# Kernel optimization log

Hardware: AMD Instinct MI355X
Metric: run time of the kernel (lower is better)

## Reference

```python
import jax, jax.numpy as jnp
import numpy as np

VOCAB = 256
H = 4096
N_LAYERS = 2


def setup_inputs() -> dict:
    key = jax.random.key(0)
    ks = jax.random.split(key, 16)
    s = 1.0 / np.sqrt(H)
    inp = jax.random.randint(ks[0], (1,), 0, VOCAB)
    hidden = jax.random.normal(ks[1], (N_LAYERS, 1, H), dtype=jnp.float32)
    emb = jax.random.normal(ks[2], (VOCAB, H), dtype=jnp.float32)
    def u(k, shape):
        return jax.random.uniform(k, shape, jnp.float32, -s, s)
    return {
        'inp': inp,
        'hidden': hidden,
        'emb': emb,
        'W_ih0': u(ks[3], (3 * H, H)), 'W_hh0': u(ks[4], (3 * H, H)),
        'b_ih0': u(ks[5], (3 * H,)),   'b_hh0': u(ks[6], (3 * H,)),
        'W_ih1': u(ks[7], (3 * H, H)), 'W_hh1': u(ks[8], (3 * H, H)),
        'b_ih1': u(ks[9], (3 * H,)),   'b_hh1': u(ks[10], (3 * H,)),
        'W_dec': u(ks[11], (VOCAB, H)), 'b_dec': u(ks[12], (VOCAB,)),
    }


def _gru_cell(x, h, W_ih, W_hh, b_ih, b_hh):
    # x, h: [1, H]; PyTorch GRU gate math (gate order r, z, n)
    gi = x @ W_ih.T + b_ih  # [1, 3H]
    gh = h @ W_hh.T + b_hh  # [1, 3H]
    i_r, i_z, i_n = jnp.split(gi, 3, axis=-1)
    h_r, h_z, h_n = jnp.split(gh, 3, axis=-1)
    r = jax.nn.sigmoid(i_r + h_r)
    z = jax.nn.sigmoid(i_z + h_z)
    n = jnp.tanh(i_n + r * h_n)
    return (1.0 - z) * n + z * h


def reference(inp, hidden, emb, W_ih0, W_hh0, b_ih0, b_hh0,
              W_ih1, W_hh1, b_ih1, b_hh1, W_dec, b_dec):
    x = emb[inp]  # [1, H] embedding lookup (encoder)
    params = ((W_ih0, W_hh0, b_ih0, b_hh0), (W_ih1, W_hh1, b_ih1, b_hh1))
    new_h = []
    for l in range(N_LAYERS):
        h = _gru_cell(x, hidden[l], *params[l])  # [1, H]
        new_h.append(h)
        x = h  # output of layer l feeds layer l+1
    output = x @ W_dec.T + b_dec  # [1, VOCAB]
    return output, jnp.stack(new_h, axis=0)
```

## Files before the change

kernel.cpp:

```cpp
#include <hip/hip_runtime.h>

#define H 4096
#define NVOCAB 256

__device__ __forceinline__ float row_dot(const float* __restrict__ wrow,
                                         const float* __restrict__ vec,
                                         int lane) {
    const float4* wr = reinterpret_cast<const float4*>(wrow);
    const float4* xr = reinterpret_cast<const float4*>(vec);
    float acc = 0.f;
#pragma unroll
    for (int it = 0; it < 16; ++it) {
        int idx = it * 64 + lane;
        float4 w = wr[idx];
        float4 x = xr[idx];
        acc += w.x * x.x + w.y * x.y + w.z * x.z + w.w * x.w;
    }
#pragma unroll
    for (int off = 32; off > 0; off >>= 1) acc += __shfl_down(acc, off, 64);
    return acc;
}

__global__ __launch_bounds__(384) void gru_layer_kernel(
    const float* __restrict__ Wih,
    const float* __restrict__ Whh,
    const float* __restrict__ bih,
    const float* __restrict__ bhh,
    const float* __restrict__ xbase,
    const int* __restrict__ inp, int use_inp,
    const float* __restrict__ hprev,
    float* __restrict__ hout)
{
    __shared__ float lds[6];
    const int wave = threadIdx.x >> 6;
    const int lane = threadIdx.x & 63;
    const int i    = blockIdx.x;

    const float* x = xbase + (use_inp ? (size_t)inp[0] * H : 0);
    const int g = (wave < 3) ? wave : (wave - 3);
    const float* W    = (wave < 3) ? Wih : Whh;
    const float* vec  = (wave < 3) ? x   : hprev;
    const float* bias = (wave < 3) ? bih : bhh;

    float acc = row_dot(W + (size_t)(g * H + i) * H, vec, lane);
    if (lane == 0) lds[wave] = acc + bias[g * H + i];
    __syncthreads();

    if (threadIdx.x == 0) {
        float ir = lds[0], iz = lds[1], inn = lds[2];
        float hr = lds[3], hz = lds[4], hn  = lds[5];
        float r = 1.f / (1.f + __expf(-(ir + hr)));
        float z = 1.f / (1.f + __expf(-(iz + hz)));
        float n = tanhf(inn + r * hn);
        float h = hprev[i];
        hout[i] = (1.f - z) * n + z * h;
    }
}

__global__ __launch_bounds__(256) void dec_kernel(
    const float* __restrict__ Wdec,
    const float* __restrict__ bdec,
    const float* __restrict__ vec,
    float* __restrict__ out)
{
    const int wave = threadIdx.x >> 6;
    const int lane = threadIdx.x & 63;
    const int row = blockIdx.x * 4 + wave;
    float acc = row_dot(Wdec + (size_t)row * H, vec, lane);
    if (lane == 0) out[row] = acc + bdec[row];
}

extern "C" void kernel_launch(void* const* d_in, const int* in_sizes, int n_in,
                              void* d_out, int out_size, void* d_ws, size_t ws_size,
                              hipStream_t stream) {
    const int*   inp    = (const int*)d_in[0];
    const float* hidden = (const float*)d_in[1];
    const float* emb    = (const float*)d_in[2];
    const float* Wih0   = (const float*)d_in[3];
    const float* Whh0   = (const float*)d_in[4];
    const float* bih0   = (const float*)d_in[5];
    const float* bhh0   = (const float*)d_in[6];
    const float* Wih1   = (const float*)d_in[7];
    const float* Whh1   = (const float*)d_in[8];
    const float* bih1   = (const float*)d_in[9];
    const float* bhh1   = (const float*)d_in[10];
    const float* Wdec   = (const float*)d_in[11];
    const float* bdec   = (const float*)d_in[12];

    float* out = (float*)d_out;
    float* h0o = out + NVOCAB;
    float* h1o = out + NVOCAB + H;

    gru_layer_kernel<<<H, 384, 0, stream>>>(
        Wih0, Whh0, bih0, bhh0, emb, inp, 1, hidden, h0o);
    gru_layer_kernel<<<H, 384, 0, stream>>>(
        Wih1, Whh1, bih1, bhh1, h0o, inp, 0, hidden + H, h1o);
    dec_kernel<<<NVOCAB / 4, 256, 0, stream>>>(Wdec, bdec, h1o, out);
}
```

Baseline: 637.0 us.

## Process 8 hidden units per GRU block and keep input vector in registers

```diff
diff --git a/kernel.cpp b/kernel.cpp
--- a/kernel.cpp
+++ b/kernel.cpp
@@ -2,26 +2,9 @@
 
 #define H 4096
 #define NVOCAB 256
+#define NE 8
 
-__device__ __forceinline__ float row_dot(const float* __restrict__ wrow,
-                                         const float* __restrict__ vec,
-                                         int lane) {
-    const float4* wr = reinterpret_cast<const float4*>(wrow);
-    const float4* xr = reinterpret_cast<const float4*>(vec);
-    float acc = 0.f;
-#pragma unroll
-    for (int it = 0; it < 16; ++it) {
-        int idx = it * 64 + lane;
-        float4 w = wr[idx];
-        float4 x = xr[idx];
-        acc += w.x * x.x + w.y * x.y + w.z * x.z + w.w * x.w;
-    }
-#pragma unroll
-    for (int off = 32; off > 0; off >>= 1) acc += __shfl_down(acc, off, 64);
-    return acc;
-}
-
-__global__ __launch_bounds__(384) void gru_layer_kernel(
+__global__ __launch_bounds__(384, 3) void gru_layer_kernel(
     const float* __restrict__ Wih,
     const float* __restrict__ Whh,
     const float* __restrict__ bih,
@@ -31,10 +14,10 @@
     const float* __restrict__ hprev,
     float* __restrict__ hout)
 {
-    __shared__ float lds[6];
+    __shared__ float part[6][NE];
     const int wave = threadIdx.x >> 6;
     const int lane = threadIdx.x & 63;
-    const int i    = blockIdx.x;
+    const int i0   = blockIdx.x * NE;
 
     const float* x = xbase + (use_inp ? (size_t)inp[0] * H : 0);
     const int g = (wave < 3) ? wave : (wave - 3);
@@ -42,13 +25,42 @@
     const float* vec  = (wave < 3) ? x   : hprev;
     const float* bias = (wave < 3) ? bih : bhh;
 
-    float acc = row_dot(W + (size_t)(g * H + i) * H, vec, lane);
-    if (lane == 0) lds[wave] = acc + bias[g * H + i];
+    const float4* xr = reinterpret_cast<const float4*>(vec);
+    float4 v[16];
+#pragma unroll
+    for (int it = 0; it < 16; ++it) v[it] = xr[it * 64 + lane];
+
+    for (int e = 0; e < NE; ++e) {
+        const int i = i0 + e;
+        const float4* wr =
+            reinterpret_cast<const float4*>(W + (size_t)(g * H + i) * H);
+        float ax = 0.f, ay = 0.f, az = 0.f, aw = 0.f;
+#pragma unroll
+        for (int half = 0; half < 2; ++half) {
+            float4 w[8];
+#pragma unroll
+            for (int j = 0; j < 8; ++j)
+                w[j] = wr[half * 512 + j * 64 + lane];
+#pragma unroll
+            for (int j = 0; j < 8; ++j) {
+                ax += w[j].x * v[half * 8 + j].x;
+                ay += w[j].y * v[half * 8 + j].y;
+                az += w[j].z * v[half * 8 + j].z;
+                aw += w[j].w * v[half * 8 + j].w;
+            }
+        }
+        float acc = (ax + ay) + (az + aw);
+#pragma unroll
+        for (int off = 32; off > 0; off >>= 1) acc += __shfl_down(acc, off, 64);
+        if (lane == 0) part[wave][e] = acc + bias[g * H + i];
+    }
     __syncthreads();
 
-    if (threadIdx.x == 0) {
-        float ir = lds[0], iz = lds[1], inn = lds[2];
-        float hr = lds[3], hz = lds[4], hn  = lds[5];
+    if (threadIdx.x < NE) {
+        const int e = threadIdx.x;
+        const int i = i0 + e;
+        float ir = part[0][e], iz = part[1][e], inn = part[2][e];
+        float hr = part[3][e], hz = part[4][e], hn  = part[5][e];
         float r = 1.f / (1.f + __expf(-(ir + hr)));
         float z = 1.f / (1.f + __expf(-(iz + hz)));
         float n = tanhf(inn + r * hn);
@@ -66,7 +78,28 @@
     const int wave = threadIdx.x >> 6;
     const int lane = threadIdx.x & 63;
     const int row = blockIdx.x * 4 + wave;
-    float acc = row_dot(Wdec + (size_t)row * H, vec, lane);
+    const float4* wr = reinterpret_cast<const float4*>(Wdec + (size_t)row * H);
+    const float4* xr = reinterpret_cast<const float4*>(vec);
+    float ax = 0.f, ay = 0.f, az = 0.f, aw = 0.f;
+#pragma unroll
+    for (int q = 0; q < 2; ++q) {
+        float4 w[8], xv[8];
+#pragma unroll
+        for (int j = 0; j < 8; ++j) {
+            w[j]  = wr[q * 512 + j * 64 + lane];
+            xv[j] = xr[q * 512 + j * 64 + lane];
+        }
+#pragma unroll
+        for (int j = 0; j < 8; ++j) {
+            ax += w[j].x * xv[j].x;
+            ay += w[j].y * xv[j].y;
+            az += w[j].z * xv[j].z;
+            aw += w[j].w * xv[j].w;
+        }
+    }
+    float acc = (ax + ay) + (az + aw);
+#pragma unroll
+    for (int off = 32; off > 0; off >>= 1) acc += __shfl_down(acc, off, 64);
     if (lane == 0) out[row] = acc + bdec[row];
 }
 
@@ -91,9 +124,9 @@
     float* h0o = out + NVOCAB;
     float* h1o = out + NVOCAB + H;
 
-    gru_layer_kernel<<<H, 384, 0, stream>>>(
+    gru_layer_kernel<<<H / NE, 384, 0, stream>>>(
         Wih0, Whh0, bih0, bhh0, emb, inp, 1, hidden, h0o);
-    gru_layer_kernel<<<H, 384, 0, stream>>>(
+    gru_layer_kernel<<<H / NE, 384, 0, stream>>>(
         Wih1, Whh1, bih1, bhh1, h0o, inp, 0, hidden + H, h1o);
     dec_kernel<<<NVOCAB / 4, 256, 0, stream>>>(Wdec, bdec, h1o, out);
 }
```

Result: no change. 641.1 us (+0.6%).
